# Kernel optimization log

Measured on AMD Instinct MI355X. Metric: run time of the kernel, lower is better.

Reference implementation:

```python
import jax, jax.numpy as jnp
import numpy as np

D = 1024      # embedding_dim
H = 16        # num_heads
DH = D // H   # head_dim
DFF = 4 * D
EPS = 1e-5


def setup_inputs() -> dict:
    key = jax.random.key(0)
    ks = jax.random.split(key, 10)
    B, T = 2, 2048
    s = 0.02
    return {
        "x": jax.random.normal(ks[0], (B, T, D), dtype=jnp.float32),
        "Wq": jax.random.normal(ks[1], (H, D, DH), dtype=jnp.float32) * s,
        "Wk": jax.random.normal(ks[2], (H, D, DH), dtype=jnp.float32) * s,
        "Wv": jax.random.normal(ks[3], (H, D, DH), dtype=jnp.float32) * s,
        "W1": jax.random.normal(ks[4], (D, DFF), dtype=jnp.float32) * s,
        "b1": jnp.zeros((DFF,), dtype=jnp.float32),
        "W2": jax.random.normal(ks[5], (DFF, D), dtype=jnp.float32) * s,
        "b2": jnp.zeros((D,), dtype=jnp.float32),
        "gamma1": jnp.ones((D,), dtype=jnp.float32),
        "beta1": jnp.zeros((D,), dtype=jnp.float32),
        "gamma2": jnp.ones((D,), dtype=jnp.float32),
        "beta2": jnp.zeros((D,), dtype=jnp.float32),
    }


def _layernorm(x, gamma, beta):
    # torch.var default is unbiased (ddof=1) -- faithful to LayerNorm1d
    mean = jnp.mean(x, axis=-1, keepdims=True)
    var = jnp.var(x, axis=-1, keepdims=True, ddof=1)
    return gamma * (x - mean) * jax.lax.rsqrt(var + EPS) + beta


def _block(x, Wq, Wk, Wv, W1, b1, W2, b2, gamma1, beta1, gamma2, beta2):
    B, T, _ = x.shape
    h = _layernorm(x, gamma1, beta1)
    # per-head projections stacked: [B,H,T,DH]
    Q = jnp.einsum('btd,hde->bhte', h, Wq)
    K = jnp.einsum('btd,hde->bhte', h, Wk)
    V = jnp.einsum('btd,hde->bhte', h, Wv)
    # NOTE: original scales by 1/sqrt(embedding_dim), NOT head_dim
    scores = jnp.einsum('bhqe,bhke->bhqk', Q, K) / jnp.sqrt(jnp.float32(D))
    causal = jnp.tril(jnp.ones((T, T), dtype=bool))
    scores = jnp.where(causal, scores, -jnp.inf)
    attn = jax.nn.softmax(scores, axis=-1)
    out = jnp.einsum('bhqk,bhke->bhqe', attn, V)
    # torch.cat over heads along last dim == transpose+reshape
    out = out.transpose(0, 2, 1, 3).reshape(B, T, D)
    x = x + out
    h2 = _layernorm(x, gamma2, beta2)
    ff = jax.nn.relu(h2 @ W1 + b1) @ W2 + b2  # dropout is identity at inference
    return x + ff


def reference(x, Wq, Wk, Wv, W1, b1, W2, b2, gamma1, beta1, gamma2, beta2):
    return _block(x, Wq, Wk, Wv, W1, b1, W2, b2, gamma1, beta1, gamma2, beta2)
```

## Files before the change

kernel.cpp:

```cpp
#include <hip/hip_runtime.h>

typedef unsigned short u16;
typedef __bf16 bf16;
typedef __attribute__((ext_vector_type(8))) __bf16 bf16x8;
typedef __attribute__((ext_vector_type(4))) float f32x4;
typedef __attribute__((ext_vector_type(8))) unsigned short u16x8;
typedef unsigned long long u64;

__device__ __forceinline__ float bf2f(u16 h) {
  return __uint_as_float(((unsigned int)h) << 16);
}
__device__ __forceinline__ u16 f2bf(float f) {
  unsigned int u = __float_as_uint(f);
  return (u16)((u + 0x7fffu + ((u >> 16) & 1u)) >> 16);
}
__device__ __forceinline__ u16 ld_cv(const void* p, size_t i, int f32) {
  return f32 ? f2bf(((const float*)p)[i]) : ((const u16*)p)[i];
}
__device__ __forceinline__ float ld_f(const void* p, size_t i, int f32) {
  return f32 ? ((const float*)p)[i] : bf2f(((const u16*)p)[i]);
}
__device__ __forceinline__ void async16(const u16* g, u16* l) {
  __builtin_amdgcn_global_load_lds(
      (const __attribute__((address_space(1))) unsigned int*)g,
      (__attribute__((address_space(3))) unsigned int*)l, 16, 0, 0);
}
__device__ __forceinline__ unsigned pk_bf16(float hi, float lo) {
  return __builtin_amdgcn_perm(__float_as_uint(hi) + 0x8000u,
                               __float_as_uint(lo) + 0x8000u, 0x07060302u);
}

__global__ void sniff_kernel(const u16* __restrict__ x, int* __restrict__ flag) {
  const int tid = threadIdx.x;
  int me = 0;
#pragma unroll
  for (int j = 0; j < 4; j++) {
    const u16 v = x[(tid * 4 + j) * 2];
    const int e = (v >> 7) & 0xFF;
    me = me > e ? me : e;
  }
#pragma unroll
  for (int off = 32; off > 0; off >>= 1) {
    const int o = __shfl_down(me, off);
    me = me > o ? me : o;
  }
  __shared__ int sm[4];
  if ((tid & 63) == 0) sm[tid >> 6] = me;
  __syncthreads();
  if (tid == 0) {
    int a = sm[0] > sm[1] ? sm[0] : sm[1];
    int b = sm[2] > sm[3] ? sm[2] : sm[3];
    *flag = ((a > b ? a : b) >= 140) ? 1 : 0;
  }
}

__global__ void prep_kernel(const void* __restrict__ Wq, const void* __restrict__ Wk,
                            const void* __restrict__ Wv, const void* __restrict__ W1,
                            const void* __restrict__ W2,
                            u16* __restrict__ WTq, u16* __restrict__ W1T,
                            u16* __restrict__ W2T, const int* __restrict__ flag) {
  __shared__ u16 tile[64][65];
  const int f = *flag;
  const int bid = blockIdx.x;
  const int lx = threadIdx.x & 63, ly = threadIdx.x >> 6;
  if (bid < 768) {
    const int bx = bid & 15, wh = bid >> 4;
    const int w = wh >> 4, hh = wh & 15;
    const int tr = bx * 64;
    const void* W = (w == 0) ? Wq : ((w == 1) ? Wk : Wv);
    const size_t hbase = (size_t)hh * 65536;
#pragma unroll
    for (int i = 0; i < 16; i++)
      tile[ly * 16 + i][lx] = ld_cv(W, hbase + (size_t)(tr + ly * 16 + i) * 64 + lx, f);
    __syncthreads();
#pragma unroll
    for (int i = 0; i < 16; i++)
      WTq[((size_t)(w * 1024 + hh * 64 + ly * 16 + i)) * 1024 + tr + lx] =
          tile[lx][ly * 16 + i];
  } else {
    const void* src;
    u16* dst;
    int R, C, tc, tr;
    if (bid < 1792) {
      const int j = bid - 768;
      src = W1; dst = W1T; R = 1024; C = 4096;
      tc = (j & 63) * 64; tr = (j >> 6) * 64;
    } else {
      const int j = bid - 1792;
      src = W2; dst = W2T; R = 4096; C = 1024;
      tc = (j & 15) * 64; tr = (j >> 4) * 64;
    }
#pragma unroll
    for (int i = 0; i < 16; i++)
      tile[ly * 16 + i][lx] = ld_cv(src, (size_t)(tr + ly * 16 + i) * C + tc + lx, f);
    __syncthreads();
#pragma unroll
    for (int i = 0; i < 16; i++)
      dst[(size_t)(tc + ly * 16 + i) * R + tr + lx] = tile[lx][ly * 16 + i];
  }
}

template <int EPI, int WR, int WC, bool MS>
__launch_bounds__(WR * WC * 64)
__global__ void gemm_bt(const u16* __restrict__ A, const u16* __restrict__ B,
                        int K, int KLD, int NX, int N,
                        const void* __restrict__ bias, const u16* __restrict__ res,
                        void* __restrict__ out,
                        u16* __restrict__ Qo, u16* __restrict__ Ko, u16* __restrict__ Vto,
                        const int* __restrict__ flag) {
  constexpr int BM = WR * 64, BN = WC * 64, T = WR * WC * 64;
  constexpr int RPA = T / 4;
  constexpr int RAH = BM / RPA;
  constexpr int RBH = BN / RPA;
  __shared__ __align__(16) u16 As[BM * 64];
  __shared__ __align__(16) u16 Bs[BN * 64];
  const int tid = threadIdx.x;
  const int bid = blockIdx.x;
  const int sxp = NX >> 3;
  const int xcd = bid & 7, j9 = bid >> 3;
  int m0, n0, koff = 0, khb = 0;
  if (EPI == 3) {
    m0 = (xcd * 4 + (j9 & 3)) * BM;
    n0 = ((j9 >> 2) & 7) * BN;
    khb = (j9 >> 5) & 1;
    koff = khb * K;
  } else if (MS) {
    m0 = (xcd * sxp + j9 % sxp) * BM;
    n0 = (j9 / sxp) * BN;
  } else {
    n0 = (xcd * sxp + j9 % sxp) * BN;
    m0 = (j9 / sxp) * BM;
  }
  const int wave = tid >> 6, lane = tid & 63;
  const int wm = (wave / WC) * 64, wn = (wave % WC) * 64;
  const int lm = lane & 15, lq = lane >> 4;
  const int fb = (EPI == 1 || EPI == 2) ? *flag : 0;

  const f32x4 zero = {0.f, 0.f, 0.f, 0.f};
  f32x4 acc[4][4];
#pragma unroll
  for (int i = 0; i < 4; i++)
#pragma unroll
    for (int j = 0; j < 4; j++) acc[i][j] = zero;

  const int ar = tid >> 2;
  const int ac = (tid & 3) * 8;
  const u16* Ag = A + (size_t)(m0 + ar) * KLD + koff + ac;
  const u16* Bg = B + (size_t)(n0 + ar) * KLD + koff + ac;
  u16* AsP = &As[tid * 8];
  u16* BsP = &Bs[tid * 8];

  for (int k0 = 0; k0 < K; k0 += 64) {
#pragma unroll
    for (int hh = 0; hh < 2; hh++) {
#pragma unroll
      for (int c = 0; c < RAH; c++)
        async16(Ag + k0 + hh * 32 + (size_t)c * RPA * KLD,
                AsP + hh * BM * 32 + c * RPA * 32);
#pragma unroll
      for (int c = 0; c < RBH; c++)
        async16(Bg + k0 + hh * 32 + (size_t)c * RPA * KLD,
                BsP + hh * BN * 32 + c * RPA * 32);
    }
    __syncthreads();
    bf16x8 a0[4], a1[4], b0[4], b1[4];
#pragma unroll
    for (int i = 0; i < 4; i++) {
      a0[i] = *(const bf16x8*)&As[(wm + i * 16 + lm) * 32 + lq * 8];
      a1[i] = *(const bf16x8*)&As[BM * 32 + (wm + i * 16 + lm) * 32 + lq * 8];
    }
#pragma unroll
    for (int i = 0; i < 4; i++) {
      b0[i] = *(const bf16x8*)&Bs[(wn + i * 16 + lm) * 32 + lq * 8];
      b1[i] = *(const bf16x8*)&Bs[BN * 32 + (wn + i * 16 + lm) * 32 + lq * 8];
    }
#pragma unroll
    for (int i = 0; i < 4; i++)
#pragma unroll
      for (int j = 0; j < 4; j++) {
        acc[i][j] = __builtin_amdgcn_mfma_f32_16x16x32_bf16(a0[i], b0[j], acc[i][j], 0, 0, 0);
        acc[i][j] = __builtin_amdgcn_mfma_f32_16x16x32_bf16(a1[i], b1[j], acc[i][j], 0, 0, 0);
      }
    __syncthreads();
  }

  if (EPI == 0) {
#pragma unroll
    for (int i = 0; i < 4; i++) {
      const int row0 = m0 + wm + i * 16 + lq * 4;
      const int bb = row0 >> 11, t0 = row0 & 2047;
#pragma unroll
      for (int j = 0; j < 4; j++) {
        const int col = n0 + wn + j * 16 + lm;
        const int w = col >> 10, nn = col & 1023;
        const int hh = nn >> 6, e = nn & 63;
        if (w == 2) {
          ushort4 v4;
          v4.x = f2bf(acc[i][j][0]);
          v4.y = f2bf(acc[i][j][1]);
          v4.z = f2bf(acc[i][j][2]);
          v4.w = f2bf(acc[i][j][3]);
          *(ushort4*)&Vto[(((size_t)(bb * 16 + hh)) * 64 + e) * 2048 + t0] = v4;
        } else {
          u16* dst = (w == 0) ? Qo : Ko;
#pragma unroll
          for (int r = 0; r < 4; r++)
            dst[(((size_t)(bb * 16 + hh)) * 2048 + t0 + r) * 64 + e] =
                f2bf(acc[i][j][r]);
        }
      }
    }
  } else if (EPI == 3) {
    u16* P = khb ? Ko : Qo;
#pragma unroll
    for (int i = 0; i < 4; i++) {
#pragma unroll
      for (int r = 0; r < 4; r++) {
        const int row = m0 + wm + i * 16 + lq * 4 + r;
#pragma unroll
        for (int j = 0; j < 4; j++) {
          const int col = n0 + wn + j * 16 + lm;
          P[(size_t)row * N + col] = f2bf(acc[i][j][r]);
        }
      }
    }
  } else {
#pragma unroll
    for (int i = 0; i < 4; i++) {
#pragma unroll
      for (int r = 0; r < 4; r++) {
        const int row = m0 + wm + i * 16 + lq * 4 + r;
#pragma unroll
        for (int j = 0; j < 4; j++) {
          const int col = n0 + wn + j * 16 + lm;
          const float c = acc[i][j][r];
          if (EPI == 1) {
            const float v = c + ld_f(bias, col, fb);
            ((u16*)out)[(size_t)row * N + col] = f2bf(v > 0.f ? v : 0.f);
          } else {
            const float v = c + ld_f(bias, col, fb) + bf2f(res[(size_t)row * N + col]);
            if (fb)
              ((float*)out)[(size_t)row * N + col] = v;
            else
              ((u16*)out)[(size_t)row * N + col] = f2bf(v);
          }
        }
      }
    }
  }
}

__launch_bounds__(256)
__global__ void ffn2_reduce(const u16* __restrict__ P0, const u16* __restrict__ P1,
                            const void* __restrict__ bias, const u16* __restrict__ res,
                            void* __restrict__ out, const int* __restrict__ flag) {
  const int f = *flag;
  const size_t i0 = ((size_t)blockIdx.x * 256 + threadIdx.x) * 8;
  const int col = (int)(i0 & 1023);
  const u16x8 a8 = *(const u16x8*)(P0 + i0);
  const u16x8 b8 = *(const u16x8*)(P1 + i0);
  const u16x8 r8 = *(const u16x8*)(res + i0);
  float v[8];
#pragma unroll
  for (int k = 0; k < 8; k++)
    v[k] = bf2f(a8[k]) + bf2f(b8[k]) + ld_f(bias, col + k, f) + bf2f(r8[k]);
  if (f) {
    float4 o0 = {v[0], v[1], v[2], v[3]};
    float4 o1 = {v[4], v[5], v[6], v[7]};
    *(float4*)((float*)out + i0) = o0;
    *(float4*)((float*)out + i0 + 4) = o1;
  } else {
    u16x8 o8;
#pragma unroll
    for (int k = 0; k < 8; k++) o8[k] = f2bf(v[k]);
    *(u16x8*)((u16*)out + i0) = o8;
  }
}

__launch_bounds__(256)
__global__ void attn_mfma(const u16* __restrict__ Q, const u16* __restrict__ K,
                          const u16* __restrict__ Vt, const void* __restrict__ xres,
                          const int* __restrict__ flag, u16* __restrict__ x2) {
  __shared__ __align__(16) unsigned char smem[35328];
  const int tid = threadIdx.x;
  const int wave = tid >> 6, lane = tid & 63;
  const int lm = lane & 15, quad = lane >> 4;
  const int bid = blockIdx.x;
  const int xcd = bid & 7, jj = bid >> 3;
  const int bh = xcd + 8 * (jj & 3);
  const int pair = jj >> 2;
  const int b = bh >> 4, h = bh & 15;
  const int f32in = *flag;

  u16* stw = (u16*)smem + wave * 4096;
  u16* Ksw = stw;
  u16* Vsw = stw + 2048;
  float (*Olds)[32][68] = (float(*)[32][68])smem;
  float (*Llds)[2][16] = (float(*)[2][16])(smem + 34816);

  const u16* Kbh = K + (size_t)bh * 131072;
  const u16* Vbh = Vt + (size_t)bh * 131072;
  const f32x4 zero = {0.f, 0.f, 0.f, 0.f};
  const int srow = lane >> 2;
  const int sch2 = (((lane & 3) ^ ((srow >> 1) & 3))) * 8;
  const int rk = (lm >> 1) & 3;

  union V8 { bf16x8 v; struct { u64 lo, hi; } q; };

#pragma unroll 1
  for (int phase = 0; phase < 2; phase++) {
    const int qb = phase ? (63 - pair) : pair;
    const int qw0 = qb * 32;

    bf16x8 qf[2][2];
#pragma unroll
    for (int s = 0; s < 2; s++) {
      const u16* Qp = Q + ((size_t)bh * 2048 + qw0 + s * 16 + lm) * 64 + quad * 8;
      qf[s][0] = *(const bf16x8*)Qp;
      qf[s][1] = *(const bf16x8*)(Qp + 32);
    }
    f32x4 ot[2][4];
#pragma unroll
    for (int s = 0; s < 2; s++)
#pragma unroll
      for (int j = 0; j < 4; j++) ot[s][j] = zero;
    float l[2] = {0.f, 0.f};

    const int nt = qb + 1;
    const int si = (nt * wave) >> 2;
    const int ei = (nt * (wave + 1)) >> 2;

    for (int t = si; t < ei; t++) {
      const int ks = t * 32;
#pragma unroll
      for (int hh2 = 0; hh2 < 2; hh2++)
#pragma unroll
        for (int c = 0; c < 2; c++)
          async16(Kbh + (size_t)(ks + c * 16 + srow) * 64 + hh2 * 32 + sch2,
                  Ksw + hh2 * 1024 + c * 512 + lane * 8);
#pragma unroll
      for (int c = 0; c < 4; c++)
        async16(Vbh + (size_t)(c * 16 + srow) * 2048 + ks + sch2,
                Vsw + c * 512 + lane * 8);
      __builtin_amdgcn_s_waitcnt(0x0F70);

      f32x4 S[2][2];
#pragma unroll
      for (int s = 0; s < 2; s++)
#pragma unroll
        for (int hh = 0; hh < 2; hh++) {
          const bf16x8 k0 =
              *(const bf16x8*)&Ksw[(hh * 16 + lm) * 32 + (quad ^ rk) * 8];
          const bf16x8 k1 =
              *(const bf16x8*)&Ksw[1024 + (hh * 16 + lm) * 32 + (quad ^ rk) * 8];
          f32x4 a = zero;
          a = __builtin_amdgcn_mfma_f32_16x16x32_bf16(k0, qf[s][0], a, 0, 0, 0);
          a = __builtin_amdgcn_mfma_f32_16x16x32_bf16(k1, qf[s][1], a, 0, 0, 0);
          S[s][hh] = a;
        }
      const bool maskT = (t == qb);
#pragma unroll
      for (int s = 0; s < 2; s++) {
        float p[2][4];
#pragma unroll
        for (int hh = 0; hh < 2; hh++)
#pragma unroll
          for (int r = 0; r < 4; r++) {
            float v = __expf(S[s][hh][r] * 0.03125f);
            if (maskT && (hh * 16 + quad * 4 + r > s * 16 + lm)) v = 0.f;
            l[s] += v;
            p[hh][r] = v;
          }
        unsigned pk[4];
        pk[0] = pk_bf16(p[0][1], p[0][0]);
        pk[1] = pk_bf16(p[0][3], p[0][2]);
        pk[2] = pk_bf16(p[1][1], p[1][0]);
        pk[3] = pk_bf16(p[1][3], p[1][2]);
        const bf16x8 pf = *(const bf16x8*)pk;
#pragma unroll
        for (int j = 0; j < 4; j++) {
          V8 vf;
          vf.q.lo = *(const u64*)&Vsw[(j * 16 + lm) * 32 +
                                      (((quad >> 1)) ^ rk) * 8 + (quad & 1) * 4];
          vf.q.hi = *(const u64*)&Vsw[(j * 16 + lm) * 32 +
                                      (((quad >> 1) | 2) ^ rk) * 8 + (quad & 1) * 4];
          ot[s][j] = __builtin_amdgcn_mfma_f32_16x16x32_bf16(vf.v, pf, ot[s][j], 0, 0, 0);
        }
      }
    }

#pragma unroll
    for (int s = 0; s < 2; s++) {
      l[s] += __shfl_xor(l[s], 16);
      l[s] += __shfl_xor(l[s], 32);
    }

    __syncthreads();

#pragma unroll
    for (int s = 0; s < 2; s++)
#pragma unroll
      for (int j = 0; j < 4; j++)
        *(f32x4*)&Olds[wave][s * 16 + lm][j * 16 + quad * 4] = ot[s][j];
    if (quad == 0) {
      Llds[wave][0][lm] = l[0];
      Llds[wave][1][lm] = l[1];
    }
    __syncthreads();
    const int q = tid >> 3;
    const int e0 = (tid & 7) * 8;
    f32x4 oa = zero, ob = zero;
#pragma unroll
    for (int w = 0; w < 4; w++) {
      oa += *(const f32x4*)&Olds[w][q][e0];
      ob += *(const f32x4*)&Olds[w][q][e0 + 4];
    }
    const float lt = Llds[0][q >> 4][q & 15] + Llds[1][q >> 4][q & 15] +
                     Llds[2][q >> 4][q & 15] + Llds[3][q >> 4][q & 15];
    const float linv = 1.f / lt;
    const size_t rowbase = ((size_t)(b * 2048 + qw0 + q)) * 1024 + h * 64 + e0;
    float xv[8];
    if (f32in) {
      const float* xf = (const float*)xres + rowbase;
      const float4 u0 = *(const float4*)xf;
      const float4 u1 = *(const float4*)(xf + 4);
      xv[0] = u0.x; xv[1] = u0.y; xv[2] = u0.z; xv[3] = u0.w;
      xv[4] = u1.x; xv[5] = u1.y; xv[6] = u1.z; xv[7] = u1.w;
    } else {
      const u16x8 u = *(const u16x8*)((const u16*)xres + rowbase);
#pragma unroll
      for (int k = 0; k < 8; k++) xv[k] = bf2f(u[k]);
    }
    u16x8 o8;
#pragma unroll
    for (int k = 0; k < 4; k++) o8[k] = f2bf(xv[k] + oa[k] * linv);
#pragma unroll
    for (int k = 0; k < 4; k++) o8[4 + k] = f2bf(xv[4 + k] + ob[k] * linv);
    *(u16x8*)&x2[rowbase] = o8;
    __syncthreads();
  }
}

__launch_bounds__(256)
__global__ void ln_kernel(const void* __restrict__ x, const void* __restrict__ gamma,
                          const void* __restrict__ beta, u16* __restrict__ out,
                          const int* __restrict__ flag, int xraw) {
  const size_t row = blockIdx.x;
  const int tid = threadIdx.x;
  const int f = *flag;
  const int fx = xraw ? f : 0;
  float v0, v1, v2, v3;
  if (fx) {
    const float4 v = *((const float4*)x + row * 256 + tid);
    v0 = v.x; v1 = v.y; v2 = v.z; v3 = v.w;
  } else {
    const ushort4 u = *((const ushort4*)x + row * 256 + tid);
    v0 = bf2f(u.x); v1 = bf2f(u.y); v2 = bf2f(u.z); v3 = bf2f(u.w);
  }
  float s = v0 + v1 + v2 + v3;
  float sq = v0 * v0 + v1 * v1 + v2 * v2 + v3 * v3;
#pragma unroll
  for (int off = 32; off > 0; off >>= 1) {
    s += __shfl_down(s, off);
    sq += __shfl_down(sq, off);
  }
  __shared__ float ss[4], ssq[4];
  if ((tid & 63) == 0) { ss[tid >> 6] = s; ssq[tid >> 6] = sq; }
  __syncthreads();
  s = ss[0] + ss[1] + ss[2] + ss[3];
  sq = ssq[0] + ssq[1] + ssq[2] + ssq[3];
  const float mean = s * (1.f / 1024.f);
  const float var = (sq - 1024.f * mean * mean) * (1.f / 1023.f);
  const float rs = rsqrtf(var + 1e-5f);
  const int c0 = tid * 4;
  ushort4 o;
  o.x = f2bf(ld_f(gamma, c0 + 0, f) * (v0 - mean) * rs + ld_f(beta, c0 + 0, f));
  o.y = f2bf(ld_f(gamma, c0 + 1, f) * (v1 - mean) * rs + ld_f(beta, c0 + 1, f));
  o.z = f2bf(ld_f(gamma, c0 + 2, f) * (v2 - mean) * rs + ld_f(beta, c0 + 2, f));
  o.w = f2bf(ld_f(gamma, c0 + 3, f) * (v3 - mean) * rs + ld_f(beta, c0 + 3, f));
  *(ushort4*)&out[row * 1024 + tid * 4] = o;
}

extern "C" void kernel_launch(void* const* d_in, const int* in_sizes, int n_in,
                              void* d_out, int out_size, void* d_ws, size_t ws_size,
                              hipStream_t stream) {
  const void* x      = d_in[0];
  const void* Wq     = d_in[1];
  const void* Wk     = d_in[2];
  const void* Wv     = d_in[3];
  const void* W1     = d_in[4];
  const void* b1     = d_in[5];
  const void* W2     = d_in[6];
  const void* b2     = d_in[7];
  const void* gamma1 = d_in[8];
  const void* beta1  = d_in[9];
  const void* gamma2 = d_in[10];
  const void* beta2  = d_in[11];
  u16* ws = (u16*)d_ws;

  const size_t M4 = 4194304;
  u16* h   = ws;
  u16* Qb  = ws + 1 * M4;
  u16* Kb  = ws + 2 * M4;
  u16* Vtb = ws + 3 * M4;
  u16* WTq = ws + 4 * M4;
  u16* x2  = ws + 4 * M4;
  u16* h2  = ws + 5 * M4;
  u16* W1T = ws + 6 * M4;
  u16* W2T = ws + 7 * M4;
  u16* ff1 = ws;
  u16* P0  = ws + 5 * M4;
  u16* P1  = ws + 6 * M4;
  int* flag = (int*)(ws + 8 * M4 + 9216);

  sniff_kernel<<<1, 256, 0, stream>>>((const u16*)x, flag);
  prep_kernel<<<2816, 256, 0, stream>>>(Wq, Wk, Wv, W1, W2, WTq, W1T, W2T, flag);
  ln_kernel<<<4096, 256, 0, stream>>>(x, gamma1, beta1, h, flag, 1);
  gemm_bt<0, 4, 2, false><<<384, 512, 0, stream>>>(h, WTq, 1024, 1024, 24, 3072,
                                                   nullptr, nullptr, nullptr,
                                                   Qb, Kb, Vtb, flag);
  attn_mfma<<<1024, 256, 0, stream>>>(Qb, Kb, Vtb, x, flag, x2);
  ln_kernel<<<4096, 256, 0, stream>>>(x2, gamma2, beta2, h2, flag, 0);
  gemm_bt<1, 4, 2, false><<<512, 512, 0, stream>>>(h2, W1T, 1024, 1024, 32, 4096,
                                                   b1, nullptr, ff1,
                                                   nullptr, nullptr, nullptr, flag);
  gemm_bt<3, 2, 2, false><<<512, 256, 0, stream>>>(ff1, W2T, 2048, 4096, 8, 1024,
                                                   nullptr, nullptr, nullptr,
                                                   P0, P1, nullptr, flag);
  ffn2_reduce<<<2048, 256, 0, stream>>>(P0, P1, b2, x2, d_out, flag);
}
```

Measured before the change: 323.6 us.

## Double-buffer attention K/V staging and swizzle GEMM LDS layout

The attention kernel now keeps two per-wave K/V staging buffers and prefetches the next tile while computing the current one, waiting only on the older loads. LDS grows to about 66KB, which may reduce occupancy. The GEMM global-to-LDS load and fragment reads use an XOR swizzle to avoid LDS bank conflicts. It also adds s_setprio around the MFMA sections and splits the causal masking out of the exp loop.

```diff
diff --git a/kernel.cpp b/kernel.cpp
--- a/kernel.cpp
+++ b/kernel.cpp
@@ -144,11 +144,12 @@
     for (int j = 0; j < 4; j++) acc[i][j] = zero;
 
   const int ar = tid >> 2;
-  const int ac = (tid & 3) * 8;
+  const int ac = ((tid & 3) ^ ((tid >> 3) & 3)) * 8;
   const u16* Ag = A + (size_t)(m0 + ar) * KLD + koff + ac;
   const u16* Bg = B + (size_t)(n0 + ar) * KLD + koff + ac;
   u16* AsP = &As[tid * 8];
   u16* BsP = &Bs[tid * 8];
+  const int rq = (lq ^ ((lm >> 1) & 3)) * 8;
 
   for (int k0 = 0; k0 < K; k0 += 64) {
 #pragma unroll
@@ -166,13 +167,13 @@
     bf16x8 a0[4], a1[4], b0[4], b1[4];
 #pragma unroll
     for (int i = 0; i < 4; i++) {
-      a0[i] = *(const bf16x8*)&As[(wm + i * 16 + lm) * 32 + lq * 8];
-      a1[i] = *(const bf16x8*)&As[BM * 32 + (wm + i * 16 + lm) * 32 + lq * 8];
+      a0[i] = *(const bf16x8*)&As[(wm + i * 16 + lm) * 32 + rq];
+      a1[i] = *(const bf16x8*)&As[BM * 32 + (wm + i * 16 + lm) * 32 + rq];
     }
 #pragma unroll
     for (int i = 0; i < 4; i++) {
-      b0[i] = *(const bf16x8*)&Bs[(wn + i * 16 + lm) * 32 + lq * 8];
-      b1[i] = *(const bf16x8*)&Bs[BN * 32 + (wn + i * 16 + lm) * 32 + lq * 8];
+      b0[i] = *(const bf16x8*)&Bs[(wn + i * 16 + lm) * 32 + rq];
+      b1[i] = *(const bf16x8*)&Bs[BN * 32 + (wn + i * 16 + lm) * 32 + rq];
     }
 #pragma unroll
     for (int i = 0; i < 4; i++)
@@ -281,7 +282,7 @@
 __global__ void attn_mfma(const u16* __restrict__ Q, const u16* __restrict__ K,
                           const u16* __restrict__ Vt, const void* __restrict__ xres,
                           const int* __restrict__ flag, u16* __restrict__ x2) {
-  __shared__ __align__(16) unsigned char smem[35328];
+  __shared__ __align__(16) unsigned char smem[66048];
   const int tid = threadIdx.x;
   const int wave = tid >> 6, lane = tid & 63;
   const int lm = lane & 15, quad = lane >> 4;
@@ -292,20 +293,32 @@
   const int b = bh >> 4, h = bh & 15;
   const int f32in = *flag;
 
-  u16* stw = (u16*)smem + wave * 4096;
-  u16* Ksw = stw;
-  u16* Vsw = stw + 2048;
+  u16* stw = (u16*)smem + wave * 8192;
   float (*Olds)[32][68] = (float(*)[32][68])smem;
-  float (*Llds)[2][16] = (float(*)[2][16])(smem + 34816);
+  float (*Llds)[2][16] = (float(*)[2][16])(smem + 65536);
 
   const u16* Kbh = K + (size_t)bh * 131072;
   const u16* Vbh = Vt + (size_t)bh * 131072;
   const f32x4 zero = {0.f, 0.f, 0.f, 0.f};
   const int srow = lane >> 2;
-  const int sch2 = (((lane & 3) ^ ((srow >> 1) & 3))) * 8;
+  const int sch2 = ((lane & 3) ^ ((srow >> 1) & 3)) * 8;
   const int rk = (lm >> 1) & 3;
 
   union V8 { bf16x8 v; struct { u64 lo, hi; } q; };
+
+  auto stageKV = [&](int t, u16* buf) {
+    const int ks = t * 32;
+#pragma unroll
+    for (int hh2 = 0; hh2 < 2; hh2++)
+#pragma unroll
+      for (int c = 0; c < 2; c++)
+        async16(Kbh + (size_t)(ks + c * 16 + srow) * 64 + hh2 * 32 + sch2,
+                buf + hh2 * 1024 + c * 512 + lane * 8);
+#pragma unroll
+    for (int c = 0; c < 4; c++)
+      async16(Vbh + (size_t)(c * 16 + srow) * 2048 + ks + sch2,
+              buf + 2048 + c * 512 + lane * 8);
+  };
 
 #pragma unroll 1
   for (int phase = 0; phase < 2; phase++) {
@@ -330,21 +343,21 @@
     const int si = (nt * wave) >> 2;
     const int ei = (nt * (wave + 1)) >> 2;
 
+    if (si < ei) stageKV(si, stw);
+
+#pragma unroll 1
     for (int t = si; t < ei; t++) {
-      const int ks = t * 32;
-#pragma unroll
-      for (int hh2 = 0; hh2 < 2; hh2++)
-#pragma unroll
-        for (int c = 0; c < 2; c++)
-          async16(Kbh + (size_t)(ks + c * 16 + srow) * 64 + hh2 * 32 + sch2,
-                  Ksw + hh2 * 1024 + c * 512 + lane * 8);
-#pragma unroll
-      for (int c = 0; c < 4; c++)
-        async16(Vbh + (size_t)(c * 16 + srow) * 2048 + ks + sch2,
-                Vsw + c * 512 + lane * 8);
-      __builtin_amdgcn_s_waitcnt(0x0F70);
+      const u16* Ksw = stw + ((t - si) & 1) * 4096;
+      const u16* Vsw = Ksw + 2048;
+      if (t + 1 < ei) {
+        stageKV(t + 1, stw + ((t - si + 1) & 1) * 4096);
+        asm volatile("s_waitcnt vmcnt(8)" ::: "memory");
+      } else {
+        asm volatile("s_waitcnt vmcnt(0)" ::: "memory");
+      }
 
       f32x4 S[2][2];
+      __builtin_amdgcn_s_setprio(1);
 #pragma unroll
       for (int s = 0; s < 2; s++)
 #pragma unroll
@@ -358,6 +371,8 @@
           a = __builtin_amdgcn_mfma_f32_16x16x32_bf16(k1, qf[s][1], a, 0, 0, 0);
           S[s][hh] = a;
         }
+      __builtin_amdgcn_s_setprio(0);
+
       const bool maskT = (t == qb);
 #pragma unroll
       for (int s = 0; s < 2; s++) {
@@ -365,18 +380,26 @@
 #pragma unroll
         for (int hh = 0; hh < 2; hh++)
 #pragma unroll
-          for (int r = 0; r < 4; r++) {
-            float v = __expf(S[s][hh][r] * 0.03125f);
-            if (maskT && (hh * 16 + quad * 4 + r > s * 16 + lm)) v = 0.f;
-            l[s] += v;
-            p[hh][r] = v;
-          }
+          for (int r = 0; r < 4; r++)
+            p[hh][r] = __expf(S[s][hh][r] * 0.03125f);
+        if (maskT) {
+#pragma unroll
+          for (int hh = 0; hh < 2; hh++)
+#pragma unroll
+            for (int r = 0; r < 4; r++)
+              if (hh * 16 + quad * 4 + r > s * 16 + lm) p[hh][r] = 0.f;
+        }
+#pragma unroll
+        for (int hh = 0; hh < 2; hh++)
+#pragma unroll
+          for (int r = 0; r < 4; r++) l[s] += p[hh][r];
         unsigned pk[4];
         pk[0] = pk_bf16(p[0][1], p[0][0]);
         pk[1] = pk_bf16(p[0][3], p[0][2]);
         pk[2] = pk_bf16(p[1][1], p[1][0]);
         pk[3] = pk_bf16(p[1][3], p[1][2]);
         const bf16x8 pf = *(const bf16x8*)pk;
+        __builtin_amdgcn_s_setprio(1);
 #pragma unroll
         for (int j = 0; j < 4; j++) {
           V8 vf;
@@ -386,6 +409,7 @@
                                       (((quad >> 1) | 2) ^ rk) * 8 + (quad & 1) * 4];
           ot[s][j] = __builtin_amdgcn_mfma_f32_16x16x32_bf16(vf.v, pf, ot[s][j], 0, 0, 0);
         }
+        __builtin_amdgcn_s_setprio(0);
       }
     }
 
```

Result: no change. 325.2 us (+0.5%).

## Swizzle GEMM LDS tiles and load attention K/V directly into registers

Applied to the files above, without the earlier changes.

The GEMM kernel now XOR-swizzles the column chunk used for its async global-to-LDS copies and for its fragment reads, to cut LDS bank conflicts. The attention kernel drops its per-wave LDS staging of K and V tiles and loads the MFMA fragments straight from global memory into registers. It also raises wave priority around the MFMA sections with s_setprio. Register-direct loads avoid the LDS round trip and the waitcnt stall, but give up the coalesced async copies, and the V reads become scattered 8-byte accesses.

```diff
diff --git a/kernel.cpp b/kernel.cpp
--- a/kernel.cpp
+++ b/kernel.cpp
@@ -144,11 +144,12 @@
     for (int j = 0; j < 4; j++) acc[i][j] = zero;
 
   const int ar = tid >> 2;
-  const int ac = (tid & 3) * 8;
+  const int ac = ((tid & 3) ^ ((tid >> 3) & 3)) * 8;
   const u16* Ag = A + (size_t)(m0 + ar) * KLD + koff + ac;
   const u16* Bg = B + (size_t)(n0 + ar) * KLD + koff + ac;
   u16* AsP = &As[tid * 8];
   u16* BsP = &Bs[tid * 8];
+  const int rq = (lq ^ ((lm >> 1) & 3)) * 8;
 
   for (int k0 = 0; k0 < K; k0 += 64) {
 #pragma unroll
@@ -166,13 +167,13 @@
     bf16x8 a0[4], a1[4], b0[4], b1[4];
 #pragma unroll
     for (int i = 0; i < 4; i++) {
-      a0[i] = *(const bf16x8*)&As[(wm + i * 16 + lm) * 32 + lq * 8];
-      a1[i] = *(const bf16x8*)&As[BM * 32 + (wm + i * 16 + lm) * 32 + lq * 8];
+      a0[i] = *(const bf16x8*)&As[(wm + i * 16 + lm) * 32 + rq];
+      a1[i] = *(const bf16x8*)&As[BM * 32 + (wm + i * 16 + lm) * 32 + rq];
     }
 #pragma unroll
     for (int i = 0; i < 4; i++) {
-      b0[i] = *(const bf16x8*)&Bs[(wn + i * 16 + lm) * 32 + lq * 8];
-      b1[i] = *(const bf16x8*)&Bs[BN * 32 + (wn + i * 16 + lm) * 32 + lq * 8];
+      b0[i] = *(const bf16x8*)&Bs[(wn + i * 16 + lm) * 32 + rq];
+      b1[i] = *(const bf16x8*)&Bs[BN * 32 + (wn + i * 16 + lm) * 32 + rq];
     }
 #pragma unroll
     for (int i = 0; i < 4; i++)
@@ -282,6 +283,8 @@
                           const u16* __restrict__ Vt, const void* __restrict__ xres,
                           const int* __restrict__ flag, u16* __restrict__ x2) {
   __shared__ __align__(16) unsigned char smem[35328];
+  float (*Olds)[32][68] = (float(*)[32][68])smem;
+  float (*Llds)[2][16] = (float(*)[2][16])(smem + 34816);
   const int tid = threadIdx.x;
   const int wave = tid >> 6, lane = tid & 63;
   const int lm = lane & 15, quad = lane >> 4;
@@ -292,18 +295,9 @@
   const int b = bh >> 4, h = bh & 15;
   const int f32in = *flag;
 
-  u16* stw = (u16*)smem + wave * 4096;
-  u16* Ksw = stw;
-  u16* Vsw = stw + 2048;
-  float (*Olds)[32][68] = (float(*)[32][68])smem;
-  float (*Llds)[2][16] = (float(*)[2][16])(smem + 34816);
-
   const u16* Kbh = K + (size_t)bh * 131072;
   const u16* Vbh = Vt + (size_t)bh * 131072;
   const f32x4 zero = {0.f, 0.f, 0.f, 0.f};
-  const int srow = lane >> 2;
-  const int sch2 = (((lane & 3) ^ ((srow >> 1) & 3))) * 8;
-  const int rk = (lm >> 1) & 3;
 
   union V8 { bf16x8 v; struct { u64 lo, hi; } q; };
 
@@ -330,38 +324,39 @@
     const int si = (nt * wave) >> 2;
     const int ei = (nt * (wave + 1)) >> 2;
 
+#pragma unroll 1
     for (int t = si; t < ei; t++) {
       const int ks = t * 32;
-#pragma unroll
-      for (int hh2 = 0; hh2 < 2; hh2++)
-#pragma unroll
-        for (int c = 0; c < 2; c++)
-          async16(Kbh + (size_t)(ks + c * 16 + srow) * 64 + hh2 * 32 + sch2,
-                  Ksw + hh2 * 1024 + c * 512 + lane * 8);
-#pragma unroll
-      for (int c = 0; c < 4; c++)
-        async16(Vbh + (size_t)(c * 16 + srow) * 2048 + ks + sch2,
-                Vsw + c * 512 + lane * 8);
-      __builtin_amdgcn_s_waitcnt(0x0F70);
-
+      V8 vf[4];
+#pragma unroll
+      for (int j = 0; j < 4; j++) {
+        const u16* Vr = Vbh + (size_t)(j * 16 + lm) * 2048 + ks + quad * 4;
+        vf[j].q.lo = *(const u64*)Vr;
+        vf[j].q.hi = *(const u64*)(Vr + 16);
+      }
+      bf16x8 kk[2][2];
+#pragma unroll
+      for (int hh = 0; hh < 2; hh++) {
+        const u16* Kr = Kbh + (size_t)(ks + hh * 16 + lm) * 64 + quad * 8;
+        kk[hh][0] = *(const bf16x8*)Kr;
+        kk[hh][1] = *(const bf16x8*)(Kr + 32);
+      }
       f32x4 S[2][2];
+      __builtin_amdgcn_s_setprio(1);
 #pragma unroll
       for (int s = 0; s < 2; s++)
 #pragma unroll
         for (int hh = 0; hh < 2; hh++) {
-          const bf16x8 k0 =
-              *(const bf16x8*)&Ksw[(hh * 16 + lm) * 32 + (quad ^ rk) * 8];
-          const bf16x8 k1 =
-              *(const bf16x8*)&Ksw[1024 + (hh * 16 + lm) * 32 + (quad ^ rk) * 8];
           f32x4 a = zero;
-          a = __builtin_amdgcn_mfma_f32_16x16x32_bf16(k0, qf[s][0], a, 0, 0, 0);
-          a = __builtin_amdgcn_mfma_f32_16x16x32_bf16(k1, qf[s][1], a, 0, 0, 0);
+          a = __builtin_amdgcn_mfma_f32_16x16x32_bf16(kk[hh][0], qf[s][0], a, 0, 0, 0);
+          a = __builtin_amdgcn_mfma_f32_16x16x32_bf16(kk[hh][1], qf[s][1], a, 0, 0, 0);
           S[s][hh] = a;
         }
+      __builtin_amdgcn_s_setprio(0);
       const bool maskT = (t == qb);
 #pragma unroll
       for (int s = 0; s < 2; s++) {
-        float p[2][4];
+        float pv[2][4];
 #pragma unroll
         for (int hh = 0; hh < 2; hh++)
 #pragma unroll
@@ -369,23 +364,19 @@
             float v = __expf(S[s][hh][r] * 0.03125f);
             if (maskT && (hh * 16 + quad * 4 + r > s * 16 + lm)) v = 0.f;
             l[s] += v;
-            p[hh][r] = v;
+            pv[hh][r] = v;
           }
         unsigned pk[4];
-        pk[0] = pk_bf16(p[0][1], p[0][0]);
-        pk[1] = pk_bf16(p[0][3], p[0][2]);
-        pk[2] = pk_bf16(p[1][1], p[1][0]);
-        pk[3] = pk_bf16(p[1][3], p[1][2]);
+        pk[0] = pk_bf16(pv[0][1], pv[0][0]);
+        pk[1] = pk_bf16(pv[0][3], pv[0][2]);
+        pk[2] = pk_bf16(pv[1][1], pv[1][0]);
+        pk[3] = pk_bf16(pv[1][3], pv[1][2]);
         const bf16x8 pf = *(const bf16x8*)pk;
-#pragma unroll
-        for (int j = 0; j < 4; j++) {
-          V8 vf;
-          vf.q.lo = *(const u64*)&Vsw[(j * 16 + lm) * 32 +
-                                      (((quad >> 1)) ^ rk) * 8 + (quad & 1) * 4];
-          vf.q.hi = *(const u64*)&Vsw[(j * 16 + lm) * 32 +
-                                      (((quad >> 1) | 2) ^ rk) * 8 + (quad & 1) * 4];
-          ot[s][j] = __builtin_amdgcn_mfma_f32_16x16x32_bf16(vf.v, pf, ot[s][j], 0, 0, 0);
-        }
+        __builtin_amdgcn_s_setprio(1);
+#pragma unroll
+        for (int j = 0; j < 4; j++)
+          ot[s][j] = __builtin_amdgcn_mfma_f32_16x16x32_bf16(vf[j].v, pf, ot[s][j], 0, 0, 0);
+        __builtin_amdgcn_s_setprio(0);
       }
     }
 
```

Measured after the change: 367.9 us. +13.7%, slower.
